# Kernel optimization log

Measured on AMD Instinct MI355X. Metric: run time of the kernel, lower is better.

The kernel has to match this reference:

```python
import jax, jax.numpy as jnp
import numpy as np

D_MODEL, D_STATE, D_CONV, EXPAND, DT_RANK = 1024, 16, 4, 2, 32
D_INNER = D_MODEL * EXPAND


def setup_inputs() -> dict:
    key = jax.random.key(0)
    ks = jax.random.split(key, 12)
    B, T = 4, 2048
    s_in = 1.0 / np.sqrt(D_MODEL)
    s_dt = 1.0 / np.sqrt(DT_RANK)
    s_out = 1.0 / np.sqrt(D_INNER)
    return {
        "x": jax.random.normal(ks[0], (B, T, D_MODEL), jnp.float32),
        "Wi": jax.random.uniform(ks[1], (2 * D_INNER, D_MODEL), jnp.float32, -s_in, s_in),
        "bi": jax.random.uniform(ks[2], (2 * D_INNER,), jnp.float32, -s_in, s_in),
        "conv_w": jax.random.uniform(ks[3], (D_INNER, 1, D_CONV), jnp.float32, -0.5, 0.5),
        "conv_b": jax.random.uniform(ks[4], (D_INNER,), jnp.float32, -0.5, 0.5),
        "Wdt": jax.random.uniform(ks[5], (D_INNER, DT_RANK), jnp.float32, -s_dt, s_dt),
        "bdt": jax.random.uniform(ks[6], (D_INNER,), jnp.float32, -s_dt, s_dt),
        "A_log": jnp.log(0.99 - jax.random.uniform(ks[7], (D_INNER, D_STATE), jnp.float32) * 0.01),
        "Bm": jax.random.normal(ks[8], (D_INNER, D_STATE), jnp.float32) * 0.01,
        "Cm": jax.random.normal(ks[9], (D_INNER, D_STATE), jnp.float32) * 0.01,
        "Dv": jnp.ones((D_INNER,), jnp.float32) * 0.1,
        "Wo": jax.random.uniform(ks[10], (D_MODEL, D_INNER), jnp.float32, -s_out, s_out),
        "bo": jax.random.uniform(ks[11], (D_MODEL,), jnp.float32, -s_out, s_out),
    }


def _ssm_forward(x, Wi, bi, conv_w, conv_b, Wdt, bdt, A_log, Bm, Cm, Dv, Wo, bo):
    Bb, T, _ = x.shape
    xz = x @ Wi.T + bi                      # [B,T,2*d_inner]
    x_in, z = xz[..., :D_INNER], xz[..., D_INNER:]
    # depthwise causal conv (torch pads both sides by d_conv-1 then slices [:T] == left-pad only)
    xc = jnp.transpose(x_in, (0, 2, 1))     # [B,d_inner,T]
    xc = jax.lax.conv_general_dilated(
        xc, conv_w, (1,), [(D_CONV - 1, 0)],
        dimension_numbers=("NCH", "OIH", "NCH"), feature_group_count=D_INNER)
    xc = xc + conv_b[None, :, None]
    u = jax.nn.silu(jnp.transpose(xc, (0, 2, 1)))  # [B,T,d_inner]
    dt = jax.nn.softplus(x_in[..., :DT_RANK] @ Wdt.T + bdt)  # [B,T,d_inner]
    A = -jnp.exp(A_log)                     # [d_inner,d_state]

    def step(h, inp):
        dt_t, u_t = inp                     # each [B,d_inner]
        h = h * jnp.exp(dt_t[:, :, None] * A[None]) + dt_t[:, :, None] * Bm[None] * u_t[:, :, None]
        y = jnp.einsum("bdn,dn->bd", h, Cm)
        return h, y

    h0 = jnp.zeros((Bb, D_INNER, D_STATE), x.dtype)
    _, ys = jax.lax.scan(step, h0, (jnp.swapaxes(dt, 0, 1), jnp.swapaxes(u, 0, 1)))
    out = jnp.swapaxes(ys, 0, 1) * jax.nn.silu(z)
    return out @ Wo.T + bo + x * Dv.mean()


def reference(x, Wi, bi, conv_w, conv_b, Wdt, bdt, A_log, Bm, Cm, Dv, Wo, bo):
    return _ssm_forward(x, Wi, bi, conv_w, conv_b, Wdt, bdt, A_log, Bm, Cm, Dv, Wo, bo)
```

## Files before the change

kernel.cpp:

```cpp
#include <hip/hip_runtime.h>
#include <hip/hip_bf16.h>
#include <math.h>
#include <stdint.h>


using bf16 = __hip_bfloat16;
typedef __attribute__((ext_vector_type(8))) __bf16 bf16x8;
typedef __attribute__((ext_vector_type(4))) float f32x4;

static constexpr int Bdim = 4;
static constexpr int Tdim = 2048;
static constexpr int DM   = 1024;
static constexpr int DI   = 2048;
static constexpr int DS   = 16;
static constexpr int DC   = 4;
static constexpr int DTR  = 32;
static constexpr int Mrows = Bdim * Tdim;
static constexpr int P    = 32;
static constexpr int TC2  = Tdim / P;

__device__ __forceinline__ float b2f(bf16 v) { return __bfloat162float(v); }
__device__ __forceinline__ bf16  f2b(float v) { return __float2bfloat16(v); }
__device__ __forceinline__ float silu_f(float v) { return v / (1.0f + __expf(-v)); }
__device__ __forceinline__ float softplus_f(float v) {
  return (v > 15.0f) ? v : __logf(1.0f + __expf(v));
}
__device__ __forceinline__ float bfbits2f(unsigned short u) {
  return __uint_as_float((unsigned)u << 16);
}

#define GLOAD_LDS16(gp, lp)                                                  \
  __builtin_amdgcn_global_load_lds(                                          \
      (const __attribute__((address_space(1))) uint32_t*)(gp),               \
      (__attribute__((address_space(3))) uint32_t*)(lp), 16, 0, 0)

__global__ __launch_bounds__(256)
void kmean(const float* __restrict__ Dv, float* __restrict__ meanp) {
  __shared__ float red[256];
  float s = 0.0f;
  for (int i = threadIdx.x; i < DI; i += 256) s += Dv[i];
  red[threadIdx.x] = s;
  __syncthreads();
  for (int o = 128; o > 0; o >>= 1) {
    if (threadIdx.x < o) red[threadIdx.x] += red[threadIdx.x + o];
    __syncthreads();
  }
  if (threadIdx.x == 0) *meanp = red[0] / (float)DI;
}

__device__ __forceinline__ unsigned pack2(float x, float y) {
  return (unsigned)__builtin_bit_cast(unsigned short, f2b(x)) |
         ((unsigned)__builtin_bit_cast(unsigned short, f2b(y)) << 16);
}
__global__ __launch_bounds__(256)
void kcvt(const float* __restrict__ src, bf16* __restrict__ dst, int n8) {
  const int i = blockIdx.x * 256 + threadIdx.x;
  if (i >= n8) return;
  const float4 a = reinterpret_cast<const float4*>(src)[2 * i];
  const float4 b = reinterpret_cast<const float4*>(src)[2 * i + 1];
  uint4 v;
  v.x = pack2(a.x, a.y); v.y = pack2(a.z, a.w);
  v.z = pack2(b.x, b.y); v.w = pack2(b.z, b.w);
  reinterpret_cast<uint4*>(dst)[i] = v;
}

__global__ __launch_bounds__(256)
void k1(const bf16* __restrict__ A, const bf16* __restrict__ W,
        const float* __restrict__ bi,
        bf16* __restrict__ XIN, bf16* __restrict__ ZG)
{
  __shared__ bf16 Al[128 * 32];
  __shared__ bf16 Bl[128 * 32];
  const int tid  = threadIdx.x;
  const int bm   = blockIdx.y * 128;
  const int bn   = blockIdx.x * 128;
  const int lane = tid & 63, wid = tid >> 6;
  const int wr = wid >> 1, wc = wid & 1;
  const int fr = lane & 15;
  const int kg = (lane >> 4) * 8;
  const int ldr = tid >> 2, ldc = (tid & 3) * 8;
  constexpr int K = DM;

  const bf16* ga = A + (size_t)(bm + ldr) * K + ldc;
  const bf16* gb = W + (size_t)(bn + ldr) * K + ldc;

  f32x4 acc[4][4];
#pragma unroll
  for (int i = 0; i < 4; ++i)
#pragma unroll
    for (int j = 0; j < 4; ++j) acc[i][j] = (f32x4){0.f, 0.f, 0.f, 0.f};

  for (int k0 = 0; k0 < K; k0 += 32) {
    GLOAD_LDS16(ga + k0,          &Al[tid * 8]);
    GLOAD_LDS16(ga + k0 + 64 * K, &Al[2048 + tid * 8]);
    GLOAD_LDS16(gb + k0,          &Bl[tid * 8]);
    GLOAD_LDS16(gb + k0 + 64 * K, &Bl[2048 + tid * 8]);
    asm volatile("s_waitcnt vmcnt(0)" ::: "memory");
    __syncthreads();
    bf16x8 af[4], bfr[4];
#pragma unroll
    for (int i = 0; i < 4; ++i)
      af[i]  = *(const bf16x8*)&Al[(wr * 64 + i * 16 + fr) * 32 + kg];
#pragma unroll
    for (int j = 0; j < 4; ++j)
      bfr[j] = *(const bf16x8*)&Bl[(wc * 64 + j * 16 + fr) * 32 + kg];
#pragma unroll
    for (int i = 0; i < 4; ++i)
#pragma unroll
      for (int j = 0; j < 4; ++j)
        acc[i][j] = __builtin_amdgcn_mfma_f32_16x16x32_bf16(
            af[i], bfr[j], acc[i][j], 0, 0, 0);
    __syncthreads();
  }

  const int r0 = (lane >> 4) * 4;
#pragma unroll
  for (int j = 0; j < 4; ++j) {
    const int col = bn + wc * 64 + j * 16 + fr;
    const float bv = bi[col];
    const bool isx = (col < DI);
#pragma unroll
    for (int i = 0; i < 4; ++i) {
      const int rowb = bm + wr * 64 + i * 16 + r0;
#pragma unroll
      for (int r = 0; r < 4; ++r) {
        const float v = acc[i][j][r] + bv;
        if (isx) XIN[(size_t)(rowb + r) * DI + col]        = f2b(v);
        else     ZG [(size_t)(rowb + r) * DI + (col - DI)] = f2b(silu_f(v));
      }
    }
  }
}

__global__ __launch_bounds__(256)
void kscanA(const bf16* __restrict__ XIN, const bf16* __restrict__ WDTB,
            const float* __restrict__ cw, const float* __restrict__ cb,
            const float* __restrict__ bdt,
            const float* __restrict__ A_log, const float* __restrict__ Bm,
            float* __restrict__ APROD, float* __restrict__ HEND,
            float* __restrict__ DTg, float* __restrict__ Fg)
{
  __shared__ float xc[67][20];
  __shared__ float dts[16][68];
  __shared__ float fs [16][68];

  const int tid  = threadIdx.x;
  const int lane = tid & 63;
  const int wid  = tid >> 6;
  const int n  = tid & 15;
  const int dl = tid >> 4;
  const int d0 = blockIdx.x * 16;
  const int d  = d0 + dl;
  const int row0 = blockIdx.y * 64;
  const int b  = row0 >> 11;
  const size_t rbase = (size_t)b * Tdim;
  const int t0 = row0 - (int)rbase;

  const int fr = lane & 15;
  const int kg = (lane >> 4) * 8;
  const float bdtf = bdt[d0 + fr];
  const bf16x8 wfrag = *(const bf16x8*)&WDTB[(size_t)(d0 + fr) * DTR + kg];

  const float Af = -__expf(A_log[(size_t)d * DS + n]);
  const float Bf = Bm[(size_t)d * DS + n];
  const float w0 = cw[d * DC + 0], w1 = cw[d * DC + 1];
  const float w2 = cw[d * DC + 2], w3 = cw[d * DC + 3];
  const float c0 = cb[d];

  for (int e = tid; e < 67 * 4; e += 256) {
    const int i = e >> 2, p4 = (e & 3) * 4;
    const int rr = t0 + i - 3;
    float4 v;
    if (rr < 0) {
      v = make_float4(0.f, 0.f, 0.f, 0.f);
    } else {
      const ushort4 u =
          *(const ushort4*)&XIN[(rbase + rr) * DI + d0 + p4];
      v = make_float4(bfbits2f(u.x), bfbits2f(u.y), bfbits2f(u.z), bfbits2f(u.w));
    }
    *(float4*)&xc[i][p4] = v;
  }
  {
    const bf16x8 xfrag =
        *(const bf16x8*)&XIN[(rbase + t0 + wid * 16 + fr) * DI + kg];
    f32x4 a = (f32x4){0.f, 0.f, 0.f, 0.f};
    a = __builtin_amdgcn_mfma_f32_16x16x32_bf16(xfrag, wfrag, a, 0, 0, 0);
    float4 dq;
    dq.x = softplus_f(a[0] + bdtf);
    dq.y = softplus_f(a[1] + bdtf);
    dq.z = softplus_f(a[2] + bdtf);
    dq.w = softplus_f(a[3] + bdtf);
    *(float4*)&dts[fr][wid * 16 + (lane >> 4) * 4] = dq;
  }
  __syncthreads();

#pragma unroll
  for (int q = 0; q < 4; ++q) {
    const int tl = n + 16 * q;
    const float cv = c0 + w0 * xc[tl][dl] + w1 * xc[tl + 1][dl]
                        + w2 * xc[tl + 2][dl] + w3 * xc[tl + 3][dl];
    const float uv  = silu_f(cv);
    const float dtv = dts[dl][tl];
    const float fv  = dtv * uv;
    fs[dl][tl] = fv;
    const size_t go = (size_t)(d0 + dl) * Mrows + row0 + tl;
    DTg[go] = dtv;
    Fg [go] = fv;
  }
  __syncthreads();

  float acc = 0.0f;
  float R   = 0.0f;
#pragma unroll 4
  for (int sq = 15; sq >= 0; --sq) {
    const float4 dv = *(const float4*)&dts[dl][4 * sq];
    const float4 fv = *(const float4*)&fs [dl][4 * sq];
#define ASTEP(DT, FF)                                                         \
    {                                                                         \
      acc += __expf(R * Af) * (Bf * (FF));                                    \
      R += (DT);                                                              \
    }
    ASTEP(dv.w, fv.w); ASTEP(dv.z, fv.z); ASTEP(dv.y, fv.y); ASTEP(dv.x, fv.x);
#undef ASTEP
  }

  const size_t si = (size_t)blockIdx.y * DI * DS + (size_t)d * DS + n;
  APROD[si] = __expf(R * Af);
  HEND [si] = acc;
}

__global__ __launch_bounds__(256)
void kscanH(const float* __restrict__ APROD, const float* __restrict__ HEND,
            float* __restrict__ HINIT)
{
  const int idx = blockIdx.x * 256 + threadIdx.x;
  const int b  = idx / (DI * DS);
  const int dn = idx % (DI * DS);
  float H = 0.0f;
#pragma unroll
  for (int c = 0; c < P; ++c) {
    const size_t si = (size_t)(b * P + c) * DI * DS + dn;
    HINIT[si] = H;
    H = APROD[si] * H + HEND[si];
  }
}

__global__ __launch_bounds__(256)
void kscanB(const float* __restrict__ DTg, const float* __restrict__ Fg,
            bf16* __restrict__ ZG,
            const float* __restrict__ A_log, const float* __restrict__ Bm,
            const float* __restrict__ Cm, const float* __restrict__ HINIT)
{
  __shared__ float ys[16][68];

  const int tid = threadIdx.x;
  const int n  = tid & 15;
  const int dl = tid >> 4;
  const int d0 = blockIdx.x * 16;
  const int d  = d0 + dl;
  const int row0 = blockIdx.y * 64;

  const float Af = -__expf(A_log[(size_t)d * DS + n]);
  const float Bf = Bm[(size_t)d * DS + n];
  const float Cf = Cm[(size_t)d * DS + n];

  float h = HINIT[(size_t)blockIdx.y * DI * DS + (size_t)d * DS + n];

  const size_t base = (size_t)(d0 + dl) * Mrows + row0;
  const float4* dp = (const float4*)(DTg + base);
  const float4* fp = (const float4*)(Fg  + base);

#pragma unroll 4
  for (int tq = 0; tq < 16; ++tq) {
    const float4 dv = dp[tq];
    const float4 fv = fp[tq];
    float4 y4;
#define SCAN_STEP(DT, FF, YS)                                                 \
    {                                                                         \
      h = h * __expf((DT) * Af) + Bf * (FF);                                  \
      float y = h * Cf;                                                       \
      y += __int_as_float(__builtin_amdgcn_update_dpp(                        \
               0, __float_as_int(y), 0x111, 0xf, 0xf, true));                 \
      y += __int_as_float(__builtin_amdgcn_update_dpp(                        \
               0, __float_as_int(y), 0x112, 0xf, 0xf, true));                 \
      y += __int_as_float(__builtin_amdgcn_update_dpp(                        \
               0, __float_as_int(y), 0x114, 0xf, 0xf, true));                 \
      y += __int_as_float(__builtin_amdgcn_update_dpp(                        \
               0, __float_as_int(y), 0x118, 0xf, 0xf, true));                 \
      YS = y;                                                                 \
    }
    SCAN_STEP(dv.x, fv.x, y4.x);
    SCAN_STEP(dv.y, fv.y, y4.y);
    SCAN_STEP(dv.z, fv.z, y4.z);
    SCAN_STEP(dv.w, fv.w, y4.w);
#undef SCAN_STEP
    if (n == 15) *(float4*)&ys[dl][4 * tq] = y4;
  }
  __syncthreads();

  {
    const int tl = tid >> 2, p4 = (tid & 3) * 4;
    const size_t gi = (size_t)(row0 + tl) * DI + d0 + p4;
    ushort4 zv = *(const ushort4*)&ZG[gi];
    ushort4 ov;
    ov.x = __builtin_bit_cast(unsigned short, f2b(ys[p4 + 0][tl] * bfbits2f(zv.x)));
    ov.y = __builtin_bit_cast(unsigned short, f2b(ys[p4 + 1][tl] * bfbits2f(zv.y)));
    ov.z = __builtin_bit_cast(unsigned short, f2b(ys[p4 + 2][tl] * bfbits2f(zv.z)));
    ov.w = __builtin_bit_cast(unsigned short, f2b(ys[p4 + 3][tl] * bfbits2f(zv.w)));
    *(ushort4*)&ZG[gi] = ov;
  }
}

__global__ __launch_bounds__(256)
void k2(const bf16* __restrict__ G, const bf16* __restrict__ W,
        const float* __restrict__ x, const float* __restrict__ bo,
        const float* __restrict__ meanp, float* __restrict__ out)
{
  __shared__ bf16 Al[128 * 32];
  __shared__ bf16 Bl[128 * 32];
  const int tid  = threadIdx.x;
  const int bm   = blockIdx.y * 128;
  const int bn   = blockIdx.x * 128;
  const int lane = tid & 63, wid = tid >> 6;
  const int wr = wid >> 1, wc = wid & 1;
  const int fr = lane & 15;
  const int kg = (lane >> 4) * 8;
  const int ldr = tid >> 2, ldc = (tid & 3) * 8;
  constexpr int K = DI;

  const bf16* ga = G + (size_t)(bm + ldr) * K + ldc;
  const bf16* gb = W + (size_t)(bn + ldr) * K + ldc;
  const float mv = *meanp;

  f32x4 acc[4][4];
#pragma unroll
  for (int i = 0; i < 4; ++i)
#pragma unroll
    for (int j = 0; j < 4; ++j) acc[i][j] = (f32x4){0.f, 0.f, 0.f, 0.f};

  for (int k0 = 0; k0 < K; k0 += 32) {
    GLOAD_LDS16(ga + k0,          &Al[tid * 8]);
    GLOAD_LDS16(ga + k0 + 64 * K, &Al[2048 + tid * 8]);
    GLOAD_LDS16(gb + k0,          &Bl[tid * 8]);
    GLOAD_LDS16(gb + k0 + 64 * K, &Bl[2048 + tid * 8]);
    asm volatile("s_waitcnt vmcnt(0)" ::: "memory");
    __syncthreads();
    bf16x8 af[4], bfr[4];
#pragma unroll
    for (int i = 0; i < 4; ++i)
      af[i]  = *(const bf16x8*)&Al[(wr * 64 + i * 16 + fr) * 32 + kg];
#pragma unroll
    for (int j = 0; j < 4; ++j)
      bfr[j] = *(const bf16x8*)&Bl[(wc * 64 + j * 16 + fr) * 32 + kg];
#pragma unroll
    for (int i = 0; i < 4; ++i)
#pragma unroll
      for (int j = 0; j < 4; ++j)
        acc[i][j] = __builtin_amdgcn_mfma_f32_16x16x32_bf16(
            af[i], bfr[j], acc[i][j], 0, 0, 0);
    __syncthreads();
  }

  const int r0 = (lane >> 4) * 4;
#pragma unroll
  for (int j = 0; j < 4; ++j) {
    const int col = bn + wc * 64 + j * 16 + fr;
    const float bv = bo[col];
#pragma unroll
    for (int i = 0; i < 4; ++i) {
      const int rowb = bm + wr * 64 + i * 16 + r0;
#pragma unroll
      for (int r = 0; r < 4; ++r) {
        const size_t oi = (size_t)(rowb + r) * DM + col;
        out[oi] = acc[i][j][r] + bv + mv * x[oi];
      }
    }
  }
}

extern "C" void kernel_launch(void* const* d_in, const int* in_sizes, int n_in,
                              void* d_out, int out_size, void* d_ws, size_t ws_size,
                              hipStream_t stream)
{
  const float* x    = (const float*)d_in[0];
  const float* Wi   = (const float*)d_in[1];
  const float* bi   = (const float*)d_in[2];
  const float* cw   = (const float*)d_in[3];
  const float* cb   = (const float*)d_in[4];
  const float* Wdt  = (const float*)d_in[5];
  const float* bdt  = (const float*)d_in[6];
  const float* Alog = (const float*)d_in[7];
  const float* Bm   = (const float*)d_in[8];
  const float* Cm   = (const float*)d_in[9];
  const float* Dv   = (const float*)d_in[10];
  const float* Wo   = (const float*)d_in[11];
  const float* bo   = (const float*)d_in[12];
  float* out = (float*)d_out;

  char* ws = (char*)d_ws;
  float* MEANP = (float*)(ws);
  bf16*  WOB   = (bf16*)(ws + 256);
  bf16*  XIN   = (bf16*)(ws + 4194560);
  bf16*  ZG    = (bf16*)(ws + 37748992);
  float* APROD = (float*)(ws + 71303424);
  float* HEND  = (float*)(ws + 88080640);
  float* HINIT = (float*)(ws + 104857856);
  bf16*  WDTB  = (bf16*)(ws + 121635072);
  float* DTg   = (float*)(ws + 121766144);
  bf16*  XB    = (bf16*)(ws + 121766144);
  bf16*  WIB   = (bf16*)(ws + 138543360);
  float* Fg    = (float*)(ws + 188875008);

  kmean<<<1, 256, 0, stream>>>(Dv, MEANP);
  kcvt<<<Mrows * DM / 8 / 256, 256, 0, stream>>>(x,  XB,  Mrows * DM / 8);
  kcvt<<<2 * DI * DM / 8 / 256, 256, 0, stream>>>(Wi, WIB, 2 * DI * DM / 8);
  kcvt<<<DM * DI / 8 / 256, 256, 0, stream>>>(Wo, WOB, DM * DI / 8);
  kcvt<<<DI * DTR / 8 / 256, 256, 0, stream>>>(Wdt, WDTB, DI * DTR / 8);

  k1<<<dim3(2 * DI / 128, Mrows / 128), 256, 0, stream>>>(XB, WIB, bi, XIN, ZG);

  kscanA<<<dim3(DI / 16, Mrows / 64), 256, 0, stream>>>(
      XIN, WDTB, cw, cb, bdt, Alog, Bm, APROD, HEND, DTg, Fg);
  kscanH<<<dim3(Bdim * DI * DS / 256), 256, 0, stream>>>(APROD, HEND, HINIT);
  kscanB<<<dim3(DI / 16, Mrows / 64), 256, 0, stream>>>(
      DTg, Fg, ZG, Alog, Bm, Cm, HINIT);

  k2<<<dim3(DM / 128, Mrows / 128), 256, 0, stream>>>(ZG, WOB, x, bo, MEANP, out);
}
```

Before: 480.7 us.

## Restructure chunk scan to one thread per channel with interleaved dt/f buffer

The dt and dt*u intermediates are now stored as one interleaved float2 buffer in row-major [row, channel] order instead of two channel-major arrays. The second scan pass gives each thread a whole channel with all 16 states held in registers, which removes the DPP cross-lane reductions and the shared-memory transpose. Each thread now reads and writes the gate contiguously across the warp. Exponentials use exp2 with pre-scaled A. The cost is higher register pressure from 64 per-thread state arrays and bf16 gate stores of only 2 bytes each.

```diff
diff --git a/kernel.cpp b/kernel.cpp
--- a/kernel.cpp
+++ b/kernel.cpp
@@ -18,6 +18,7 @@
 static constexpr int Mrows = Bdim * Tdim;
 static constexpr int P    = 32;
 static constexpr int TC2  = Tdim / P;
+static constexpr float LOG2E = 1.44269504f;
 
 __device__ __forceinline__ float b2f(bf16 v) { return __bfloat162float(v); }
 __device__ __forceinline__ bf16  f2b(float v) { return __float2bfloat16(v); }
@@ -27,6 +28,9 @@
 }
 __device__ __forceinline__ float bfbits2f(unsigned short u) {
   return __uint_as_float((unsigned)u << 16);
+}
+__device__ __forceinline__ float exp2_f(float v) {
+  return __builtin_amdgcn_exp2f(v);
 }
 
 #define GLOAD_LDS16(gp, lp)                                                  \
@@ -138,7 +142,7 @@
             const float* __restrict__ bdt,
             const float* __restrict__ A_log, const float* __restrict__ Bm,
             float* __restrict__ APROD, float* __restrict__ HEND,
-            float* __restrict__ DTg, float* __restrict__ Fg)
+            float2* __restrict__ DFg)
 {
   __shared__ float xc[67][20];
   __shared__ float dts[16][68];
@@ -161,8 +165,8 @@
   const float bdtf = bdt[d0 + fr];
   const bf16x8 wfrag = *(const bf16x8*)&WDTB[(size_t)(d0 + fr) * DTR + kg];
 
-  const float Af = -__expf(A_log[(size_t)d * DS + n]);
-  const float Bf = Bm[(size_t)d * DS + n];
+  const float Af2 = -__expf(A_log[(size_t)d * DS + n]) * LOG2E;
+  const float Bf  = Bm[(size_t)d * DS + n];
   const float w0 = cw[d * DC + 0], w1 = cw[d * DC + 1];
   const float w2 = cw[d * DC + 2], w3 = cw[d * DC + 3];
   const float c0 = cb[d];
@@ -200,14 +204,15 @@
     const float cv = c0 + w0 * xc[tl][dl] + w1 * xc[tl + 1][dl]
                         + w2 * xc[tl + 2][dl] + w3 * xc[tl + 3][dl];
     const float uv  = silu_f(cv);
-    const float dtv = dts[dl][tl];
-    const float fv  = dtv * uv;
-    fs[dl][tl] = fv;
-    const size_t go = (size_t)(d0 + dl) * Mrows + row0 + tl;
-    DTg[go] = dtv;
-    Fg [go] = fv;
+    fs[dl][tl] = dts[dl][tl] * uv;
   }
   __syncthreads();
+
+  for (int e = tid; e < 64 * 16; e += 256) {
+    const int tl = e >> 4, dd = e & 15;
+    DFg[(size_t)(row0 + tl) * DI + d0 + dd] =
+        make_float2(dts[dd][tl], fs[dd][tl]);
+  }
 
   float acc = 0.0f;
   float R   = 0.0f;
@@ -217,7 +222,7 @@
     const float4 fv = *(const float4*)&fs [dl][4 * sq];
 #define ASTEP(DT, FF)                                                         \
     {                                                                         \
-      acc += __expf(R * Af) * (Bf * (FF));                                    \
+      acc += exp2_f(R * Af2) * (Bf * (FF));                                   \
       R += (DT);                                                              \
     }
     ASTEP(dv.w, fv.w); ASTEP(dv.z, fv.z); ASTEP(dv.y, fv.y); ASTEP(dv.x, fv.x);
@@ -225,7 +230,7 @@
   }
 
   const size_t si = (size_t)blockIdx.y * DI * DS + (size_t)d * DS + n;
-  APROD[si] = __expf(R * Af);
+  APROD[si] = exp2_f(R * Af2);
   HEND [si] = acc;
 }
 
@@ -245,69 +250,40 @@
   }
 }
 
-__global__ __launch_bounds__(256)
-void kscanB(const float* __restrict__ DTg, const float* __restrict__ Fg,
-            bf16* __restrict__ ZG,
+__global__ __launch_bounds__(256, 4)
+void kscanB(const float2* __restrict__ DFg, bf16* __restrict__ ZG,
             const float* __restrict__ A_log, const float* __restrict__ Bm,
             const float* __restrict__ Cm, const float* __restrict__ HINIT)
 {
-  __shared__ float ys[16][68];
-
-  const int tid = threadIdx.x;
-  const int n  = tid & 15;
-  const int dl = tid >> 4;
-  const int d0 = blockIdx.x * 16;
-  const int d  = d0 + dl;
-  const int row0 = blockIdx.y * 64;
-
-  const float Af = -__expf(A_log[(size_t)d * DS + n]);
-  const float Bf = Bm[(size_t)d * DS + n];
-  const float Cf = Cm[(size_t)d * DS + n];
-
-  float h = HINIT[(size_t)blockIdx.y * DI * DS + (size_t)d * DS + n];
-
-  const size_t base = (size_t)(d0 + dl) * Mrows + row0;
-  const float4* dp = (const float4*)(DTg + base);
-  const float4* fp = (const float4*)(Fg  + base);
+  const int tid  = threadIdx.x;
+  const int cg   = blockIdx.x >> 3;
+  const int d    = ((blockIdx.x & 7) << 8) + tid;
+  const int row0 = cg * 64;
+
+  float A2[DS], Bc[DS], Cc[DS], h[DS];
+#pragma unroll
+  for (int nn = 0; nn < DS; ++nn) {
+    A2[nn] = -__expf(A_log[(size_t)d * DS + nn]) * LOG2E;
+    Bc[nn] = Bm[(size_t)d * DS + nn];
+    Cc[nn] = Cm[(size_t)d * DS + nn];
+    h [nn] = HINIT[(size_t)cg * DI * DS + (size_t)d * DS + nn];
+  }
+
+  const float2* dfp = DFg + (size_t)row0 * DI + d;
+  bf16* zp = ZG + (size_t)row0 * DI + d;
 
 #pragma unroll 4
-  for (int tq = 0; tq < 16; ++tq) {
-    const float4 dv = dp[tq];
-    const float4 fv = fp[tq];
-    float4 y4;
-#define SCAN_STEP(DT, FF, YS)                                                 \
-    {                                                                         \
-      h = h * __expf((DT) * Af) + Bf * (FF);                                  \
-      float y = h * Cf;                                                       \
-      y += __int_as_float(__builtin_amdgcn_update_dpp(                        \
-               0, __float_as_int(y), 0x111, 0xf, 0xf, true));                 \
-      y += __int_as_float(__builtin_amdgcn_update_dpp(                        \
-               0, __float_as_int(y), 0x112, 0xf, 0xf, true));                 \
-      y += __int_as_float(__builtin_amdgcn_update_dpp(                        \
-               0, __float_as_int(y), 0x114, 0xf, 0xf, true));                 \
-      y += __int_as_float(__builtin_amdgcn_update_dpp(                        \
-               0, __float_as_int(y), 0x118, 0xf, 0xf, true));                 \
-      YS = y;                                                                 \
+  for (int t = 0; t < TC2; ++t) {
+    const float2 df = dfp[(size_t)t * DI];
+    float y = 0.0f;
+#pragma unroll
+    for (int nn = 0; nn < DS; ++nn) {
+      const float e = exp2_f(df.x * A2[nn]);
+      h[nn] = h[nn] * e + Bc[nn] * df.y;
+      y += h[nn] * Cc[nn];
     }
-    SCAN_STEP(dv.x, fv.x, y4.x);
-    SCAN_STEP(dv.y, fv.y, y4.y);
-    SCAN_STEP(dv.z, fv.z, y4.z);
-    SCAN_STEP(dv.w, fv.w, y4.w);
-#undef SCAN_STEP
-    if (n == 15) *(float4*)&ys[dl][4 * tq] = y4;
-  }
-  __syncthreads();
-
-  {
-    const int tl = tid >> 2, p4 = (tid & 3) * 4;
-    const size_t gi = (size_t)(row0 + tl) * DI + d0 + p4;
-    ushort4 zv = *(const ushort4*)&ZG[gi];
-    ushort4 ov;
-    ov.x = __builtin_bit_cast(unsigned short, f2b(ys[p4 + 0][tl] * bfbits2f(zv.x)));
-    ov.y = __builtin_bit_cast(unsigned short, f2b(ys[p4 + 1][tl] * bfbits2f(zv.y)));
-    ov.z = __builtin_bit_cast(unsigned short, f2b(ys[p4 + 2][tl] * bfbits2f(zv.z)));
-    ov.w = __builtin_bit_cast(unsigned short, f2b(ys[p4 + 3][tl] * bfbits2f(zv.w)));
-    *(ushort4*)&ZG[gi] = ov;
+    bf16* zt = zp + (size_t)t * DI;
+    *zt = f2b(y * b2f(*zt));
   }
 }
 
@@ -398,18 +374,17 @@
   float* out = (float*)d_out;
 
   char* ws = (char*)d_ws;
-  float* MEANP = (float*)(ws);
-  bf16*  WOB   = (bf16*)(ws + 256);
-  bf16*  XIN   = (bf16*)(ws + 4194560);
-  bf16*  ZG    = (bf16*)(ws + 37748992);
-  float* APROD = (float*)(ws + 71303424);
-  float* HEND  = (float*)(ws + 88080640);
-  float* HINIT = (float*)(ws + 104857856);
-  bf16*  WDTB  = (bf16*)(ws + 121635072);
-  float* DTg   = (float*)(ws + 121766144);
-  bf16*  XB    = (bf16*)(ws + 121766144);
-  bf16*  WIB   = (bf16*)(ws + 138543360);
-  float* Fg    = (float*)(ws + 188875008);
+  float*  MEANP = (float*)(ws);
+  bf16*   WOB   = (bf16*)(ws + 256);
+  bf16*   XIN   = (bf16*)(ws + 4194560);
+  bf16*   ZG    = (bf16*)(ws + 37748992);
+  float*  APROD = (float*)(ws + 71303424);
+  float*  HEND  = (float*)(ws + 88080640);
+  float*  HINIT = (float*)(ws + 104857856);
+  bf16*   WDTB  = (bf16*)(ws + 121635072);
+  float2* DFg   = (float2*)(ws + 121766144);
+  bf16*   XB    = (bf16*)(ws + 121766144);
+  bf16*   WIB   = (bf16*)(ws + 138543360);
 
   kmean<<<1, 256, 0, stream>>>(Dv, MEANP);
   kcvt<<<Mrows * DM / 8 / 256, 256, 0, stream>>>(x,  XB,  Mrows * DM / 8);
@@ -420,10 +395,10 @@
   k1<<<dim3(2 * DI / 128, Mrows / 128), 256, 0, stream>>>(XB, WIB, bi, XIN, ZG);
 
   kscanA<<<dim3(DI / 16, Mrows / 64), 256, 0, stream>>>(
-      XIN, WDTB, cw, cb, bdt, Alog, Bm, APROD, HEND, DTg, Fg);
+      XIN, WDTB, cw, cb, bdt, Alog, Bm, APROD, HEND, DFg);
   kscanH<<<dim3(Bdim * DI * DS / 256), 256, 0, stream>>>(APROD, HEND, HINIT);
-  kscanB<<<dim3(DI / 16, Mrows / 64), 256, 0, stream>>>(
-      DTg, Fg, ZG, Alog, Bm, Cm, HINIT);
+  kscanB<<<dim3(Mrows / 64 * 8), 256, 0, stream>>>(
+      DFg, ZG, Alog, Bm, Cm, HINIT);
 
   k2<<<dim3(DM / 128, Mrows / 128), 256, 0, stream>>>(ZG, WOB, x, bo, MEANP, out);
 }
```

Result: faster. 427.0 us (-11.2%).
